# Kernel tuning notes

Hardware: AMD Instinct MI355X
Metric: run time of the kernel (lower is better)

The kernel has to match this reference:

```python
import jax, jax.numpy as jnp
import numpy as np

UNITS = 256
INNER_ITERS = 1
INNER_LR = [0.01]
LN_EPS = 1e-3  # keras LayerNormalization default epsilon
B, L, F = 512, 128, 128


def _encoder(W1, b1, W2, b2, z):
    # keras 'gelu' activation is exact (approximate=False)
    h = jax.nn.gelu(z @ W1 + b1, approximate=False)
    return h @ W2 + b2


def _layer_norm(z, g, b):
    m = jnp.mean(z, axis=-1, keepdims=True)
    v = jnp.var(z, axis=-1, keepdims=True)
    return g * (z - m) / jnp.sqrt(v + LN_EPS) + b


def setup_inputs():
    U = UNITS
    key = jax.random.key(0)
    ks = jax.random.split(key, 12)
    s = 0.02
    return {
        "inputs": jax.random.normal(ks[0], (B, F), jnp.float32),
        "prev_hidden": jax.random.normal(ks[1], (B, U), jnp.float32),
        "sequence_buffer": jax.random.normal(ks[2], (B, L, U), jnp.float32),
        "Wp": jax.random.normal(ks[3], (F, U)) * s, "bp": jnp.zeros((U,)),
        "Wphi": jax.random.normal(ks[4], (U, U)) * s, "bphi": jnp.zeros((U,)),
        "Wpsi": jax.random.normal(ks[5], (U, U)) * s, "bpsi": jnp.zeros((U,)),
        "W1": jax.random.normal(ks[6], (U, 4 * U)) * s, "b1": jnp.zeros((4 * U,)),
        "W2": jax.random.normal(ks[7], (4 * U, U)) * s, "b2": jnp.zeros((U,)),
        "Wg": jax.random.normal(ks[8], (U, U)) * s, "g_bias": jnp.zeros((U,)),
        "ln_g": jnp.ones((U,)), "ln_b": jnp.zeros((U,)),
        "Wh": jax.random.normal(ks[9], (U, U)) * s, "h_bias": jnp.zeros((U,)),
    }


def reference(inputs, prev_hidden, sequence_buffer, Wp, bp, Wphi, bphi, Wpsi, bpsi,
              W1, b1, W2, b2, Wg, g_bias, ln_g, ln_b, Wh, h_bias):
    U = UNITS
    bsz = inputs.shape[0]
    # input projection (F != units)
    proj = inputs @ Wp + bp                                   # [B, U]
    # shift buffer, append projected input
    buf = jnp.concatenate([sequence_buffer[:, 1:, :], proj[:, None, :]], axis=1)  # [B, L, U]
    x = buf[:, :-1, :].reshape(-1, U)                         # [B*(L-1), U]
    y = buf[:, 1:, :].reshape(-1, U)
    phi = x @ Wphi + bphi

    params = (W1, b1, W2, b2)

    def inner_loss(p):
        rec = _layer_norm(_encoder(*p, phi) @ Wg + g_bias, ln_g, ln_b)
        return jnp.mean(jnp.square(rec - y)), rec

    rec = None
    for it in range(INNER_ITERS):
        (_, rec), grads = jax.value_and_grad(inner_loss, has_aux=True)(params)
        lr = INNER_LR[min(it, len(INNER_LR) - 1)]
        params = tuple(p - lr * g for p, g in zip(params, grads))

    psi = buf[:, -1, :] @ Wpsi + bpsi                         # [B, U]
    contrib = jnp.mean(rec.reshape(bsz, -1, U), axis=1)       # [B, U]
    # psi path uses the UPDATED inner-encoder weights
    out = (_encoder(*params, psi) + contrib) @ Wh + h_bias    # [B, U]
    return out, buf
```

## Files before the change

kernel.cpp:

```cpp
#include <hip/hip_runtime.h>
#include <cmath>

typedef __bf16 bf16;
typedef __attribute__((ext_vector_type(8))) __bf16 bf16x8;
typedef __attribute__((ext_vector_type(4))) __bf16 bf16x4v;
typedef __attribute__((ext_vector_type(4))) float f32x4;
typedef __attribute__((ext_vector_type(2))) unsigned int u32x2;

constexpr int NROWS = 512 * 127;
constexpr float LR = 0.01f;
constexpr float INV_NU = 1.f / (65024.f * 256.f);

__device__ __forceinline__ float sigf(float x) {
  return 1.f / (1.f + __expf(-1.702f * x));
}
__device__ __forceinline__ float gelu_fast(float x) { return x * sigf(x); }
__device__ __forceinline__ float dgelu_fast(float x) {
  float s = sigf(x);
  return s * (1.f + 1.702f * x * (1.f - s));
}
__device__ __forceinline__ bf16x8 gelu8f(bf16x8 v) {
  bf16x8 o;
#pragma unroll
  for (int i = 0; i < 8; i++) o[i] = (bf16)gelu_fast((float)v[i]);
  return o;
}

__device__ __forceinline__ void gload16(const bf16* g, const bf16* lds) {
  __builtin_amdgcn_global_load_lds(
      (const __attribute__((address_space(1))) unsigned int*)(size_t)(const void*)g,
      (__attribute__((address_space(3))) unsigned int*)(unsigned)(size_t)(const void*)lds,
      16, 0, 0);
}

template <int EPI>
__global__ __launch_bounds__(256) void gemm3_k(
    const bf16* __restrict__ A, const bf16* __restrict__ Bt,
    const float* __restrict__ bias, void* __restrict__ out0,
    void* __restrict__ out1, const bf16* __restrict__ aux,
    int M, int N, int K) {
  __shared__ __align__(16) bf16 As[2][128 * 64];
  __shared__ __align__(16) bf16 Bs[2][128 * 64];
  const int t = threadIdx.x;
  const int bn = blockIdx.x * 128, bm = blockIdx.y * 128;
  const int lane = t & 63, w = t >> 6;
  const int wr = w >> 1, wc = w & 1;

  f32x4 acc[4][4];
#pragma unroll
  for (int mi = 0; mi < 4; mi++)
#pragma unroll
    for (int ni = 0; ni < 4; ni++) {
      f32x4 z = {0.f, 0.f, 0.f, 0.f};
      acc[mi][ni] = z;
    }

  const int l8 = lane >> 3;
  const int p = lane & 7;
  const int csw = p ^ l8;
  const bf16* aBase = A + (size_t)(bm + 32 * w + l8) * K + csw * 8;
  const bf16* bBase = Bt + (size_t)(bn + 32 * w + l8) * K + csw * 8;

  const int ml = lane & 15, g = lane >> 4;
  const int c0 = g ^ (ml & 7);
  const int c1 = (4 | g) ^ (ml & 7);

  const int nt = K >> 6;
#pragma unroll
  for (int i = 0; i < 4; i++) {
    gload16(aBase + (size_t)(8 * i) * K, As[0] + (32 * w + 8 * i) * 64);
    gload16(bBase + (size_t)(8 * i) * K, Bs[0] + (32 * w + 8 * i) * 64);
  }
  __syncthreads();

  for (int tt = 0; tt < nt; tt++) {
    const int cur = tt & 1;
    if (tt + 1 < nt) {
      const int ko = (tt + 1) * 64;
#pragma unroll
      for (int i = 0; i < 4; i++) {
        gload16(aBase + (size_t)(8 * i) * K + ko, As[cur ^ 1] + (32 * w + 8 * i) * 64);
        gload16(bBase + (size_t)(8 * i) * K + ko, Bs[cur ^ 1] + (32 * w + 8 * i) * 64);
      }
    }
    bf16x8 af[2][4], bfr[2][4];
#pragma unroll
    for (int mi = 0; mi < 4; mi++) {
      const int m = wr * 64 + mi * 16 + ml;
      const int n = wc * 64 + mi * 16 + ml;
      af[0][mi] = *(const bf16x8*)&As[cur][m * 64 + c0 * 8];
      af[1][mi] = *(const bf16x8*)&As[cur][m * 64 + c1 * 8];
      bfr[0][mi] = *(const bf16x8*)&Bs[cur][n * 64 + c0 * 8];
      bfr[1][mi] = *(const bf16x8*)&Bs[cur][n * 64 + c1 * 8];
    }
#pragma unroll
    for (int ks = 0; ks < 2; ks++)
#pragma unroll
      for (int mi = 0; mi < 4; mi++)
#pragma unroll
        for (int ni = 0; ni < 4; ni++)
          acc[mi][ni] = __builtin_amdgcn_mfma_f32_16x16x32_bf16(
              bfr[ks][ni], af[ks][mi], acc[mi][ni], 0, 0, 0);
    __syncthreads();
  }

  const int g4 = (lane >> 4) << 2;
#pragma unroll
  for (int mi = 0; mi < 4; mi++) {
    const int m = bm + wr * 64 + mi * 16 + ml;
#pragma unroll
    for (int ni = 0; ni < 4; ni++) {
      const int n0 = bn + wc * 64 + ni * 16 + g4;
      f32x4 v = acc[mi][ni];
      if (bias) {
        const float4 bv = *(const float4*)(bias + n0);
        v[0] += bv.x; v[1] += bv.y; v[2] += bv.z; v[3] += bv.w;
      }
      const size_t idx = (size_t)m * N + n0;
      if constexpr (EPI == 0) {
        *(float4*)((float*)out0 + idx) = make_float4(v[0], v[1], v[2], v[3]);
      } else if constexpr (EPI == 1) {
        bf16x4v o;
#pragma unroll
        for (int j = 0; j < 4; j++) o[j] = (bf16)v[j];
        *(bf16x4v*)((bf16*)out0 + idx) = o;
      } else if constexpr (EPI == 2) {
        bf16x4v od, oh;
#pragma unroll
        for (int j = 0; j < 4; j++) {
          float s = sigf(v[j]);
          oh[j] = (bf16)(v[j] * s);
          od[j] = (bf16)(s * (1.f + 1.702f * v[j] * (1.f - s)));
        }
        *(bf16x4v*)((bf16*)out0 + idx) = od;
        *(bf16x4v*)((bf16*)out1 + idx) = oh;
      } else if constexpr (EPI == 3) {
        bf16x4v o;
#pragma unroll
        for (int j = 0; j < 4; j++) o[j] = (bf16)gelu_fast(v[j]);
        *(bf16x4v*)((bf16*)out0 + idx) = o;
      } else if constexpr (EPI == 5) {
        const bf16x4v a4 = *(const bf16x4v*)(aux + idx);
        bf16x4v o;
#pragma unroll
        for (int j = 0; j < 4; j++) o[j] = (bf16)(v[j] * dgelu_fast((float)a4[j]));
        *(bf16x4v*)((bf16*)out0 + idx) = o;
      } else {
        const bf16x4v a4 = *(const bf16x4v*)(aux + idx);
        bf16x4v o;
#pragma unroll
        for (int j = 0; j < 4; j++) o[j] = (bf16)(v[j] * (float)a4[j]);
        *(bf16x4v*)((bf16*)out0 + idx) = o;
      }
    }
  }
}

template <int EPI, bool GA>
__global__ __launch_bounds__(256) void gemm_k(
    const bf16* __restrict__ A, const bf16* __restrict__ Bt,
    const float* __restrict__ bias, void* __restrict__ out0,
    void* __restrict__ out1, const bf16* __restrict__ aux,
    int M, int N, int K) {
  __shared__ bf16 As[128][40];
  __shared__ bf16 Bs[128][40];
  const int t = threadIdx.x;
  const int bm = blockIdx.x * 128, bn = blockIdx.y * 128;
  const int lane = t & 63, w = t >> 6;
  const int wr = w >> 1, wc = w & 1;

  f32x4 acc[4][4];
#pragma unroll
  for (int mi = 0; mi < 4; mi++)
#pragma unroll
    for (int ni = 0; ni < 4; ni++) {
      f32x4 z = {0.f, 0.f, 0.f, 0.f};
      acc[mi][ni] = z;
    }
  const int r2 = t >> 2;
  const int c8 = (t & 3) * 8;

  for (int kt = 0; kt < K; kt += 32) {
    __syncthreads();
    {
      bf16x8 a0 = *(const bf16x8*)(A + (size_t)(bm + r2) * K + kt + c8);
      bf16x8 a1 = *(const bf16x8*)(A + (size_t)(bm + r2 + 64) * K + kt + c8);
      bf16x8 b0 = *(const bf16x8*)(Bt + (size_t)(bn + r2) * K + kt + c8);
      bf16x8 b1 = *(const bf16x8*)(Bt + (size_t)(bn + r2 + 64) * K + kt + c8);
      if constexpr (GA) { a0 = gelu8f(a0); a1 = gelu8f(a1); }
      *(bf16x8*)&As[r2][c8] = a0;
      *(bf16x8*)&As[r2 + 64][c8] = a1;
      *(bf16x8*)&Bs[r2][c8] = b0;
      *(bf16x8*)&Bs[r2 + 64][c8] = b1;
    }
    __syncthreads();
    bf16x8 af[4], bfr[4];
#pragma unroll
    for (int mi = 0; mi < 4; mi++)
      af[mi] = *(const bf16x8*)&As[wr * 64 + mi * 16 + (lane & 15)][(lane >> 4) * 8];
#pragma unroll
    for (int ni = 0; ni < 4; ni++)
      bfr[ni] = *(const bf16x8*)&Bs[wc * 64 + ni * 16 + (lane & 15)][(lane >> 4) * 8];
#pragma unroll
    for (int mi = 0; mi < 4; mi++)
#pragma unroll
      for (int ni = 0; ni < 4; ni++)
        acc[mi][ni] = __builtin_amdgcn_mfma_f32_16x16x32_bf16(af[mi], bfr[ni], acc[mi][ni], 0, 0, 0);
  }

#pragma unroll
  for (int ni = 0; ni < 4; ni++) {
    const int col = bn + wc * 64 + ni * 16 + (lane & 15);
    const float bv = bias ? bias[col] : 0.f;
#pragma unroll
    for (int mi = 0; mi < 4; mi++) {
      const int rb = bm + wr * 64 + mi * 16 + ((lane >> 4) << 2);
#pragma unroll
      for (int r = 0; r < 4; r++) {
        float v = acc[mi][ni][r] + bv;
        size_t idx = (size_t)(rb + r) * N + col;
        if constexpr (EPI == 1) {
          ((bf16*)out0)[idx] = (bf16)v;
        } else {
          ((float*)out0)[idx] = v;
        }
      }
    }
  }
}

template <bool GELU_A>
__global__ __launch_bounds__(256) void tgemm3_k(
    const bf16* __restrict__ Asrc, const bf16* __restrict__ Bsrc,
    float* __restrict__ outP, int M, int N, int ldA, int ldB, int K) {
  __shared__ __align__(16) bf16 As[4736];
  __shared__ __align__(16) bf16 Bs[4736];
  const int t = threadIdx.x;
  const int bm = blockIdx.x * 128, bn = blockIdx.y * 128;
  const int r0 = blockIdx.z * 1024;
  const int rows = (K - r0 < 1024) ? (K - r0) : 1024;
  const int lane = t & 63, w = t >> 6, wr = w >> 1, wc = w & 1;

  f32x4 acc[4][4];
#pragma unroll
  for (int mi = 0; mi < 4; mi++)
#pragma unroll
    for (int ni = 0; ni < 4; ni++) {
      f32x4 z = {0.f, 0.f, 0.f, 0.f};
      acc[mi][ni] = z;
    }

  const bool isB = t >= 128;
  const int srow = (t & 127) >> 4;
  const int scol = (t & 15) * 8;
  const int sms = (t & 15) >> 1;
  const int shalf = (t & 1) * 8;
  const bf16* src = isB ? Bsrc : Asrc;
  const int ld = isB ? ldB : ldA;
  const int bx = isB ? bn : bm;
  bf16* dst = isB ? Bs : As;

  const unsigned abase = (unsigned)(size_t)(void*)As;
  const unsigned bbase = (unsigned)(size_t)(void*)Bs;
  const int g = lane >> 4;
  const int ml = lane & 15;
  const unsigned acol0 = abase + 2u * (unsigned)((wr * 4) * 592 + g * 144 + ml);
  const unsigned bcol0 = bbase + 2u * (unsigned)((wc * 4) * 592 + g * 144 + ml);

  for (int kt = 0; kt < rows; kt += 32) {
    __syncthreads();
#pragma unroll
    for (int ll = 0; ll < 4; ll++) {
      const int row = srow + ll * 8;
      bf16x8 v = *(const bf16x8*)(src + (size_t)(r0 + kt + row) * ld + bx + scol);
      if constexpr (GELU_A) { if (!isB) v = gelu8f(v); }
      *(bf16x8*)&dst[sms * 592 + ll * 144 + srow * 16 + shalf] = v;
    }
    __syncthreads();

    union FR { u32x2 p[2]; bf16x8 v; };
    FR af[4], bfr[4];
#pragma unroll
    for (int mi = 0; mi < 4; mi++) {
      const unsigned a = acol0 + (unsigned)(mi * 592 * 2);
      asm volatile("ds_read_b64_tr_b16 %0, %1" : "=v"(af[mi].p[0]) : "v"(a));
      asm volatile("ds_read_b64_tr_b16 %0, %1 offset:128" : "=v"(af[mi].p[1]) : "v"(a));
    }
#pragma unroll
    for (int ni = 0; ni < 4; ni++) {
      const unsigned b = bcol0 + (unsigned)(ni * 592 * 2);
      asm volatile("ds_read_b64_tr_b16 %0, %1" : "=v"(bfr[ni].p[0]) : "v"(b));
      asm volatile("ds_read_b64_tr_b16 %0, %1 offset:128" : "=v"(bfr[ni].p[1]) : "v"(b));
    }
    asm volatile("s_waitcnt lgkmcnt(0)" ::: "memory");
    __builtin_amdgcn_sched_barrier(0);

#pragma unroll
    for (int mi = 0; mi < 4; mi++)
#pragma unroll
      for (int ni = 0; ni < 4; ni++)
        acc[mi][ni] = __builtin_amdgcn_mfma_f32_16x16x32_bf16(
            bfr[ni].v, af[mi].v, acc[mi][ni], 0, 0, 0);
  }

  float* o = outP + (size_t)blockIdx.z * M * N;
  const int g4 = (lane >> 4) << 2;
#pragma unroll
  for (int mi = 0; mi < 4; mi++) {
    const int m = bm + wr * 64 + mi * 16 + ml;
#pragma unroll
    for (int ni = 0; ni < 4; ni++) {
      const int n0 = bn + wc * 64 + ni * 16 + g4;
      f32x4 v = acc[mi][ni];
      *(float4*)(o + (size_t)m * N + n0) = make_float4(v[0], v[1], v[2], v[3]);
    }
  }
}

__global__ void prep_k(const float* inputs, const float* Wp, const float* Wphi,
                       const float* W1, const float* W2, const float* Wg,
                       const float* Wpsi, const float* Wh,
                       bf16* inb, bf16* WpT, bf16* WphiT, bf16* W1T, bf16* W2T,
                       bf16* WgT, bf16* Wgb, bf16* W2b, bf16* WpsiT, bf16* WhT) {
  int i = blockIdx.x * 256 + threadIdx.x;
  if (i < 65536) {
    inb[i] = (bf16)inputs[i];
  } else if ((i -= 65536) < 32768) {
    int u = i >> 7, f = i & 127;
    WpT[i] = (bf16)Wp[f * 256 + u];
  } else if ((i -= 32768) < 65536) {
    int n = i >> 8, k = i & 255;
    WphiT[i] = (bf16)Wphi[k * 256 + n];
  } else if ((i -= 65536) < 262144) {
    int h = i >> 8, u = i & 255;
    W1T[i] = (bf16)W1[u * 1024 + h];
  } else if ((i -= 262144) < 262144) {
    int u = i >> 10, h = i & 1023;
    W2T[i] = (bf16)W2[h * 256 + u];
  } else if ((i -= 262144) < 65536) {
    int n = i >> 8, k = i & 255;
    WgT[i] = (bf16)Wg[k * 256 + n];
  } else if ((i -= 65536) < 65536) {
    Wgb[i] = (bf16)Wg[i];
  } else if ((i -= 65536) < 262144) {
    W2b[i] = (bf16)W2[i];
  } else if ((i -= 262144) < 65536) {
    int n = i >> 8, k = i & 255;
    WpsiT[i] = (bf16)Wpsi[k * 256 + n];
  } else if ((i -= 65536) < 65536) {
    int n = i >> 8, k = i & 255;
    WhT[i] = (bf16)Wh[k * 256 + n];
  }
}

__global__ void xcast_k(const float* __restrict__ seq, bf16* __restrict__ xb) {
  int v8 = blockIdx.x * 256 + threadIdx.x;
  int r = v8 >> 5, c8 = (v8 & 31) * 8;
  int b = r / 127, t = r - b * 127;
  const float* src = seq + ((size_t)(b * 128 + t + 1)) * 256 + c8;
  float4 v0 = *(const float4*)(src);
  float4 v1 = *(const float4*)(src + 4);
  bf16x8 o;
  o[0] = (bf16)v0.x; o[1] = (bf16)v0.y; o[2] = (bf16)v0.z; o[3] = (bf16)v0.w;
  o[4] = (bf16)v1.x; o[5] = (bf16)v1.y; o[6] = (bf16)v1.z; o[7] = (bf16)v1.w;
  *(bf16x8*)(xb + (size_t)r * 256 + c8) = o;
}

__global__ void projcast_k(const float* __restrict__ proj, bf16* __restrict__ projb) {
  int i = blockIdx.x * 256 + threadIdx.x;
  projb[i] = (bf16)proj[i];
}

__global__ void bufwrite_k(const float* __restrict__ seq, const float* __restrict__ proj,
                           float* __restrict__ buf) {
  int i = blockIdx.x * 256 + threadIdx.x;
  int b = i >> 13, rem = i & 8191;
  int j = rem >> 6, c4 = (rem & 63) * 4;
  float4 v;
  if (j < 127)
    v = *(const float4*)(seq + ((size_t)(b * 128 + j + 1)) * 256 + c4);
  else
    v = *(const float4*)(proj + (size_t)b * 256 + c4);
  *(float4*)(buf + ((size_t)(b * 128 + j)) * 256 + c4) = v;
}

__global__ __launch_bounds__(256) void ln_k(const bf16* zin, bf16* dzout,
                                            const float* __restrict__ seq,
                                            const float* __restrict__ proj,
                                            const float* __restrict__ lng,
                                            const float* __restrict__ lnb,
                                            bf16* __restrict__ rec) {
  const int w = threadIdx.x >> 6, lane = threadIdx.x & 63;
  const int r = blockIdx.x * 4 + w;
  const int b = r / 127, tt = r - b * 127;
  typedef __attribute__((ext_vector_type(4))) __bf16 bf16x4;
  bf16x4 zv = *(const bf16x4*)(zin + (size_t)r * 256 + lane * 4);
  float z0 = (float)zv[0], z1 = (float)zv[1], z2 = (float)zv[2], z3 = (float)zv[3];
  float s1 = z0 + z1 + z2 + z3;
  float s2 = z0 * z0 + z1 * z1 + z2 * z2 + z3 * z3;
  for (int m = 1; m < 64; m <<= 1) { s1 += __shfl_xor(s1, m); s2 += __shfl_xor(s2, m); }
  const float mean = s1 * (1.f / 256.f);
  const float var = s2 * (1.f / 256.f) - mean * mean;
  const float rs = rsqrtf(var + 1e-3f);
  const float4 gv = *(const float4*)(lng + lane * 4);
  const float4 bv = *(const float4*)(lnb + lane * 4);
  const float* ysrc = (tt < 126) ? (seq + ((size_t)(b * 128 + tt + 2)) * 256)
                                 : (proj + (size_t)b * 256);
  const float4 yv = *(const float4*)(ysrc + lane * 4);
  float xh0 = (z0 - mean) * rs, xh1 = (z1 - mean) * rs, xh2 = (z2 - mean) * rs, xh3 = (z3 - mean) * rs;
  float r0 = gv.x * xh0 + bv.x, r1 = gv.y * xh1 + bv.y, r2 = gv.z * xh2 + bv.z, r3 = gv.w * xh3 + bv.w;
  float u0 = 2.f * (r0 - yv.x) * INV_NU * gv.x;
  float u1 = 2.f * (r1 - yv.y) * INV_NU * gv.y;
  float u2 = 2.f * (r2 - yv.z) * INV_NU * gv.z;
  float u3 = 2.f * (r3 - yv.w) * INV_NU * gv.w;
  float t1 = u0 + u1 + u2 + u3;
  float t2 = u0 * xh0 + u1 * xh1 + u2 * xh2 + u3 * xh3;
  for (int m = 1; m < 64; m <<= 1) { t1 += __shfl_xor(t1, m); t2 += __shfl_xor(t2, m); }
  const float mu = t1 * (1.f / 256.f), mux = t2 * (1.f / 256.f);
  bf16x4 ro, dzo;
  ro[0] = (bf16)r0; ro[1] = (bf16)r1; ro[2] = (bf16)r2; ro[3] = (bf16)r3;
  dzo[0] = (bf16)((u0 - mu - xh0 * mux) * rs);
  dzo[1] = (bf16)((u1 - mu - xh1 * mux) * rs);
  dzo[2] = (bf16)((u2 - mu - xh2 * mux) * rs);
  dzo[3] = (bf16)((u3 - mu - xh3 * mux) * rs);
  *(bf16x4*)(rec + (size_t)r * 256 + lane * 4) = ro;
  *(bf16x4*)(dzout + (size_t)r * 256 + lane * 4) = dzo;
}

__global__ void colsum_k(const bf16* __restrict__ src, float* __restrict__ part, int C) {
  const int col = blockIdx.x * 256 + threadIdx.x;
  const int ch = blockIdx.y;
  float s = 0.f;
  const int rbeg = ch * 1016;
  for (int rr = rbeg; rr < rbeg + 1016; rr++) s += (float)src[(size_t)rr * C + col];
  part[(size_t)ch * C + col] = s;
}

__global__ void contrib_k(const bf16* __restrict__ rec, float* __restrict__ contrib) {
  const int b = blockIdx.x, u = threadIdx.x;
  float s = 0.f;
  for (int t = 0; t < 127; t++) s += (float)rec[((size_t)b * 127 + t) * 256 + u];
  contrib[b * 256 + u] = s * (1.f / 127.f);
}

__global__ void update2_k(const float* __restrict__ pW2, const float* __restrict__ pdb2,
                          const float* __restrict__ W2, const float* __restrict__ b2,
                          bf16* __restrict__ W2pT, float* __restrict__ b2p) {
  int idx = blockIdx.x * 256 + threadIdx.x;
  if (idx < 262144) {
    float s = 0.f;
    for (int z = 0; z < 64; z++) s += pW2[(size_t)z * 262144 + idx];
    int h = idx >> 8, u = idx & 255;
    W2pT[(size_t)u * 1024 + h] = (bf16)(W2[idx] - LR * s);
  } else {
    int u = idx - 262144;
    float s = 0.f;
    for (int c = 0; c < 64; c++) s += pdb2[c * 256 + u];
    b2p[u] = b2[u] - LR * s;
  }
}

__global__ void update1_k(const float* __restrict__ pW1, const float* __restrict__ pdb1,
                          const float* __restrict__ W1, const float* __restrict__ b1,
                          bf16* __restrict__ W1pT, float* __restrict__ b1p) {
  int idx = blockIdx.x * 256 + threadIdx.x;
  if (idx < 262144) {
    float s = 0.f;
    for (int z = 0; z < 64; z++) s += pW1[(size_t)z * 262144 + idx];
    int u = idx >> 10, h = idx & 1023;
    W1pT[(size_t)h * 256 + u] = (bf16)(W1[idx] - LR * s);
  } else {
    int h = idx - 262144;
    float s = 0.f;
    for (int c = 0; c < 64; c++) s += pdb1[c * 1024 + h];
    b1p[h] = b1[h] - LR * s;
  }
}

__global__ void fin_k(const float* __restrict__ encp, const float* __restrict__ contrib,
                      bf16* __restrict__ fin) {
  int i = blockIdx.x * 256 + threadIdx.x;
  fin[i] = (bf16)(encp[i] + contrib[i]);
}

extern "C" void kernel_launch(void* const* d_in, const int* in_sizes, int n_in,
                              void* d_out, int out_size, void* d_ws, size_t ws_size,
                              hipStream_t stream) {
  const float* inputs = (const float*)d_in[0];
  const float* seq = (const float*)d_in[2];
  const float* Wp = (const float*)d_in[3];
  const float* bp = (const float*)d_in[4];
  const float* Wphi = (const float*)d_in[5];
  const float* bphi = (const float*)d_in[6];
  const float* Wpsi = (const float*)d_in[7];
  const float* bpsi = (const float*)d_in[8];
  const float* W1 = (const float*)d_in[9];
  const float* b1 = (const float*)d_in[10];
  const float* W2 = (const float*)d_in[11];
  const float* b2 = (const float*)d_in[12];
  const float* Wg = (const float*)d_in[13];
  const float* gbias = (const float*)d_in[14];
  const float* lng = (const float*)d_in[15];
  const float* lnb = (const float*)d_in[16];
  const float* Wh = (const float*)d_in[17];
  const float* hbias = (const float*)d_in[18];

  float* out = (float*)d_out;
  float* buf = out + 131072;
  float* pW2 = buf;
  float* pW1 = buf;

  char* wptr = (char*)d_ws;
  auto alloc = [&](size_t bytes) {
    char* p = wptr;
    wptr += (bytes + 255) & ~(size_t)255;
    return p;
  };
  bf16* inb   = (bf16*)alloc(65536 * 2);
  bf16* WpT   = (bf16*)alloc(32768 * 2);
  bf16* WphiT = (bf16*)alloc(65536 * 2);
  bf16* W1T   = (bf16*)alloc(262144 * 2);
  bf16* W2T   = (bf16*)alloc(262144 * 2);
  bf16* WgT   = (bf16*)alloc(65536 * 2);
  bf16* Wgb   = (bf16*)alloc(65536 * 2);
  bf16* W2b   = (bf16*)alloc(262144 * 2);
  bf16* WpsiT = (bf16*)alloc(65536 * 2);
  bf16* WhT   = (bf16*)alloc(65536 * 2);
  bf16* W1pT  = (bf16*)alloc(262144 * 2);
  bf16* W2pT  = (bf16*)alloc(262144 * 2);
  float* b1p  = (float*)alloc(1024 * 4);
  float* b2p  = (float*)alloc(256 * 4);
  float* proj = (float*)alloc(131072 * 4);
  bf16* projb = (bf16*)alloc(131072 * 2);
  float* pdb2 = (float*)alloc(64 * 256 * 4);
  float* pdb1 = (float*)alloc(64 * 1024 * 4);
  bf16* psib  = (bf16*)alloc(131072 * 2);
  bf16* hpb   = (bf16*)alloc(524288 * 2);
  float* encp = (float*)alloc(131072 * 4);
  float* contrib = (float*)alloc(131072 * 4);
  bf16* finb  = (bf16*)alloc(131072 * 2);
  const size_t NU = (size_t)NROWS * 256;
  const size_t NH = (size_t)NROWS * 1024;
  bf16* xz     = (bf16*)alloc(NU * 2);
  bf16* phi    = (bf16*)alloc(NU * 2);
  bf16* a1b    = (bf16*)alloc(NH * 2);
  bf16* encden = (bf16*)alloc(NU * 2);
  const bool useH = ws_size >= (size_t)((char*)wptr - (char*)d_ws) + NH * 2 + 4096;
  bf16* hbuf = useH ? (bf16*)alloc(NH * 2) : nullptr;

  prep_k<<<4736, 256, 0, stream>>>(inputs, Wp, Wphi, W1, W2, Wg, Wpsi, Wh,
                                   inb, WpT, WphiT, W1T, W2T, WgT, Wgb, W2b, WpsiT, WhT);
  xcast_k<<<8128, 256, 0, stream>>>(seq, xz);
  gemm3_k<0><<<dim3(2, 4), 256, 0, stream>>>(inb, WpT, bp, proj, nullptr, nullptr, 512, 256, 128);
  projcast_k<<<512, 256, 0, stream>>>(proj, projb);
  gemm3_k<1><<<dim3(2, 508), 256, 0, stream>>>(xz, WphiT, bphi, phi, nullptr, nullptr, NROWS, 256, 256);
  if (useH)
    gemm3_k<2><<<dim3(8, 508), 256, 0, stream>>>(phi, W1T, b1, a1b, hbuf, nullptr, NROWS, 1024, 256);
  else
    gemm3_k<1><<<dim3(8, 508), 256, 0, stream>>>(phi, W1T, b1, a1b, nullptr, nullptr, NROWS, 1024, 256);
  if (useH)
    gemm3_k<1><<<dim3(2, 508), 256, 0, stream>>>(hbuf, W2T, b2, encden, nullptr, nullptr, NROWS, 256, 1024);
  else
    gemm_k<1, true><<<dim3(508, 2), 256, 0, stream>>>(a1b, W2T, b2, encden, nullptr, nullptr, NROWS, 256, 1024);
  gemm3_k<1><<<dim3(2, 508), 256, 0, stream>>>(encden, WgT, gbias, xz, nullptr, nullptr, NROWS, 256, 256);
  ln_k<<<16256, 256, 0, stream>>>(xz, xz, seq, proj, lng, lnb, encden);
  contrib_k<<<512, 256, 0, stream>>>(encden, contrib);
  gemm3_k<1><<<dim3(2, 508), 256, 0, stream>>>(xz, Wgb, nullptr, encden, nullptr, nullptr, NROWS, 256, 256);
  colsum_k<<<dim3(1, 64), 256, 0, stream>>>(encden, pdb2, 256);
  if (useH)
    tgemm3_k<false><<<dim3(8, 2, 64), 256, 0, stream>>>(hbuf, encden, pW2, 1024, 256, 1024, 256, NROWS);
  else
    tgemm3_k<true><<<dim3(8, 2, 64), 256, 0, stream>>>(a1b, encden, pW2, 1024, 256, 1024, 256, NROWS);
  update2_k<<<1025, 256, 0, stream>>>(pW2, pdb2, W2, b2, W2pT, b2p);
  if (useH)
    gemm3_k<6><<<dim3(8, 508), 256, 0, stream>>>(encden, W2b, nullptr, a1b, nullptr, a1b, NROWS, 1024, 256);
  else
    gemm3_k<5><<<dim3(8, 508), 256, 0, stream>>>(encden, W2b, nullptr, a1b, nullptr, a1b, NROWS, 1024, 256);
  colsum_k<<<dim3(4, 64), 256, 0, stream>>>(a1b, pdb1, 1024);
  tgemm3_k<false><<<dim3(2, 8, 64), 256, 0, stream>>>(phi, a1b, pW1, 256, 1024, 256, 1024, NROWS);
  update1_k<<<1028, 256, 0, stream>>>(pW1, pdb1, W1, b1, W1pT, b1p);
  bufwrite_k<<<16384, 256, 0, stream>>>(seq, proj, buf);
  gemm3_k<1><<<dim3(2, 4), 256, 0, stream>>>(projb, WpsiT, bpsi, psib, nullptr, nullptr, 512, 256, 256);
  gemm3_k<3><<<dim3(8, 4), 256, 0, stream>>>(psib, W1pT, b1p, hpb, nullptr, nullptr, 512, 1024, 256);
  gemm3_k<0><<<dim3(2, 4), 256, 0, stream>>>(hpb, W2pT, b2p, encp, nullptr, nullptr, 512, 256, 1024);
  fin_k<<<512, 256, 0, stream>>>(encp, contrib, finb);
  gemm3_k<0><<<dim3(2, 4), 256, 0, stream>>>(finb, WhT, hbias, out, nullptr, nullptr, 512, 256, 256);
}
```

Measured before the change: 944.0 us.

## Double-buffer weight-gradient GEMM loads and remap blocks across XCDs

The transposed weight-gradient GEMM (tgemm) now keeps two LDS buffers. It prefetches the next K-slice into registers while MFMAs run on the current one, which removes one barrier per iteration and hides global load latency. Both gemm3_k and the new tgemm4_k also remap the linear block index so that consecutive tiles land on the same XCD, aiming for better L2 reuse. The cost is double the LDS footprint and extra registers for the staging, which may lower occupancy.

After: 925.2 us. 1.02x faster.

```diff
diff --git a/kernel.cpp b/kernel.cpp
--- a/kernel.cpp
+++ b/kernel.cpp
@@ -31,6 +31,13 @@
       (const __attribute__((address_space(1))) unsigned int*)(size_t)(const void*)g,
       (__attribute__((address_space(3))) unsigned int*)(unsigned)(size_t)(const void*)lds,
       16, 0, 0);
+}
+
+__device__ __forceinline__ int xcd_lin() {
+  int p = ((int)blockIdx.z * (int)gridDim.y + (int)blockIdx.y) * (int)gridDim.x + (int)blockIdx.x;
+  const int total = (int)gridDim.x * (int)gridDim.y * (int)gridDim.z;
+  if (!(total & 7)) p = (p & 7) * (total >> 3) + (p >> 3);
+  return p;
 }
 
 template <int EPI>
@@ -42,7 +49,9 @@
   __shared__ __align__(16) bf16 As[2][128 * 64];
   __shared__ __align__(16) bf16 Bs[2][128 * 64];
   const int t = threadIdx.x;
-  const int bn = blockIdx.x * 128, bm = blockIdx.y * 128;
+  const int p = xcd_lin();
+  const int bn = (p % (int)gridDim.x) * 128;
+  const int bm = (p / (int)gridDim.x) * 128;
   const int lane = t & 63, w = t >> 6;
   const int wr = w >> 1, wc = w & 1;
 
@@ -56,8 +65,8 @@
     }
 
   const int l8 = lane >> 3;
-  const int p = lane & 7;
-  const int csw = p ^ l8;
+  const int pp = lane & 7;
+  const int csw = pp ^ l8;
   const bf16* aBase = A + (size_t)(bm + 32 * w + l8) * K + csw * 8;
   const bf16* bBase = Bt + (size_t)(bn + 32 * w + l8) * K + csw * 8;
 
@@ -230,15 +239,20 @@
 }
 
 template <bool GELU_A>
-__global__ __launch_bounds__(256) void tgemm3_k(
+__global__ __launch_bounds__(256) void tgemm4_k(
     const bf16* __restrict__ Asrc, const bf16* __restrict__ Bsrc,
     float* __restrict__ outP, int M, int N, int ldA, int ldB, int K) {
-  __shared__ __align__(16) bf16 As[4736];
-  __shared__ __align__(16) bf16 Bs[4736];
+  __shared__ __align__(16) bf16 As[2][4736];
+  __shared__ __align__(16) bf16 Bs[2][4736];
   const int t = threadIdx.x;
-  const int bm = blockIdx.x * 128, bn = blockIdx.y * 128;
-  const int r0 = blockIdx.z * 1024;
+  const int p = xcd_lin();
+  const int gx = (int)gridDim.x, gy = (int)gridDim.y;
+  const int bm = (p % gx) * 128;
+  const int bn = ((p / gx) % gy) * 128;
+  const int zc = p / (gx * gy);
+  const int r0 = zc * 1024;
   const int rows = (K - r0 < 1024) ? (K - r0) : 1024;
+  const int nt = rows >> 5;
   const int lane = t & 63, w = t >> 6, wr = w >> 1, wc = w & 1;
 
   f32x4 acc[4][4];
@@ -258,7 +272,7 @@
   const bf16* src = isB ? Bsrc : Asrc;
   const int ld = isB ? ldB : ldA;
   const int bx = isB ? bn : bm;
-  bf16* dst = isB ? Bs : As;
+  const int sidx = sms * 592 + srow * 16 + shalf;
 
   const unsigned abase = (unsigned)(size_t)(void*)As;
   const unsigned bbase = (unsigned)(size_t)(void*)Bs;
@@ -267,30 +281,44 @@
   const unsigned acol0 = abase + 2u * (unsigned)((wr * 4) * 592 + g * 144 + ml);
   const unsigned bcol0 = bbase + 2u * (unsigned)((wc * 4) * 592 + g * 144 + ml);
 
-  for (int kt = 0; kt < rows; kt += 32) {
-    __syncthreads();
+  auto ldrow = [&](int kt, int ll) {
+    return *(const bf16x8*)(src + (size_t)(r0 + kt + srow + ll * 8) * ld + bx + scol);
+  };
+  auto wrbuf = [&](bf16* dst, bf16x8* stg) {
 #pragma unroll
     for (int ll = 0; ll < 4; ll++) {
-      const int row = srow + ll * 8;
-      bf16x8 v = *(const bf16x8*)(src + (size_t)(r0 + kt + row) * ld + bx + scol);
+      bf16x8 v = stg[ll];
       if constexpr (GELU_A) { if (!isB) v = gelu8f(v); }
-      *(bf16x8*)&dst[sms * 592 + ll * 144 + srow * 16 + shalf] = v;
-    }
-    __syncthreads();
-
-    union FR { u32x2 p[2]; bf16x8 v; };
+      *(bf16x8*)&dst[sidx + ll * 144] = v;
+    }
+  };
+
+  bf16x8 stg[4];
+#pragma unroll
+  for (int ll = 0; ll < 4; ll++) stg[ll] = ldrow(0, ll);
+  wrbuf(isB ? Bs[0] : As[0], stg);
+  __syncthreads();
+
+  for (int tt = 0; tt < nt; tt++) {
+    const int cur = tt & 1;
+    if (tt + 1 < nt) {
+#pragma unroll
+      for (int ll = 0; ll < 4; ll++) stg[ll] = ldrow((tt + 1) * 32, ll);
+    }
+    const unsigned boff = (unsigned)cur * (4736u * 2u);
+    union FR { u32x2 pr[2]; bf16x8 v; };
     FR af[4], bfr[4];
 #pragma unroll
     for (int mi = 0; mi < 4; mi++) {
-      const unsigned a = acol0 + (unsigned)(mi * 592 * 2);
-      asm volatile("ds_read_b64_tr_b16 %0, %1" : "=v"(af[mi].p[0]) : "v"(a));
-      asm volatile("ds_read_b64_tr_b16 %0, %1 offset:128" : "=v"(af[mi].p[1]) : "v"(a));
+      const unsigned a = acol0 + boff + (unsigned)(mi * 1184);
+      asm volatile("ds_read_b64_tr_b16 %0, %1" : "=v"(af[mi].pr[0]) : "v"(a));
+      asm volatile("ds_read_b64_tr_b16 %0, %1 offset:128" : "=v"(af[mi].pr[1]) : "v"(a));
     }
 #pragma unroll
     for (int ni = 0; ni < 4; ni++) {
-      const unsigned b = bcol0 + (unsigned)(ni * 592 * 2);
-      asm volatile("ds_read_b64_tr_b16 %0, %1" : "=v"(bfr[ni].p[0]) : "v"(b));
-      asm volatile("ds_read_b64_tr_b16 %0, %1 offset:128" : "=v"(bfr[ni].p[1]) : "v"(b));
+      const unsigned b = bcol0 + boff + (unsigned)(ni * 1184);
+      asm volatile("ds_read_b64_tr_b16 %0, %1" : "=v"(bfr[ni].pr[0]) : "v"(b));
+      asm volatile("ds_read_b64_tr_b16 %0, %1 offset:128" : "=v"(bfr[ni].pr[1]) : "v"(b));
     }
     asm volatile("s_waitcnt lgkmcnt(0)" ::: "memory");
     __builtin_amdgcn_sched_barrier(0);
@@ -301,9 +329,12 @@
       for (int ni = 0; ni < 4; ni++)
         acc[mi][ni] = __builtin_amdgcn_mfma_f32_16x16x32_bf16(
             bfr[ni].v, af[mi].v, acc[mi][ni], 0, 0, 0);
-  }
-
-  float* o = outP + (size_t)blockIdx.z * M * N;
+
+    if (tt + 1 < nt) wrbuf(isB ? Bs[cur ^ 1] : As[cur ^ 1], stg);
+    __syncthreads();
+  }
+
+  float* o = outP + (size_t)zc * M * N;
   const int g4 = (lane >> 4) << 2;
 #pragma unroll
   for (int mi = 0; mi < 4; mi++) {
@@ -568,16 +599,16 @@
   gemm3_k<1><<<dim3(2, 508), 256, 0, stream>>>(xz, Wgb, nullptr, encden, nullptr, nullptr, NROWS, 256, 256);
   colsum_k<<<dim3(1, 64), 256, 0, stream>>>(encden, pdb2, 256);
   if (useH)
-    tgemm3_k<false><<<dim3(8, 2, 64), 256, 0, stream>>>(hbuf, encden, pW2, 1024, 256, 1024, 256, NROWS);
+    tgemm4_k<false><<<dim3(8, 2, 64), 256, 0, stream>>>(hbuf, encden, pW2, 1024, 256, 1024, 256, NROWS);
   else
-    tgemm3_k<true><<<dim3(8, 2, 64), 256, 0, stream>>>(a1b, encden, pW2, 1024, 256, 1024, 256, NROWS);
+    tgemm4_k<true><<<dim3(8, 2, 64), 256, 0, stream>>>(a1b, encden, pW2, 1024, 256, 1024, 256, NROWS);
   update2_k<<<1025, 256, 0, stream>>>(pW2, pdb2, W2, b2, W2pT, b2p);
   if (useH)
     gemm3_k<6><<<dim3(8, 508), 256, 0, stream>>>(encden, W2b, nullptr, a1b, nullptr, a1b, NROWS, 1024, 256);
   else
     gemm3_k<5><<<dim3(8, 508), 256, 0, stream>>>(encden, W2b, nullptr, a1b, nullptr, a1b, NROWS, 1024, 256);
   colsum_k<<<dim3(4, 64), 256, 0, stream>>>(a1b, pdb1, 1024);
-  tgemm3_k<false><<<dim3(2, 8, 64), 256, 0, stream>>>(phi, a1b, pW1, 256, 1024, 256, 1024, NROWS);
+  tgemm4_k<false><<<dim3(2, 8, 64), 256, 0, stream>>>(phi, a1b, pW1, 256, 1024, 256, 1024, NROWS);
   update1_k<<<1028, 256, 0, stream>>>(pW1, pdb1, W1, b1, W1pT, b1p);
   bufwrite_k<<<16384, 256, 0, stream>>>(seq, proj, buf);
   gemm3_k<1><<<dim3(2, 4), 256, 0, stream>>>(projb, WpsiT, bpsi, psib, nullptr, nullptr, 512, 256, 256);
```
